# Optimization experiments

Measured on AMD Instinct MI355X. Metric: run time of the kernel, lower is better.

The kernel has to match this reference:

```python
import jax, jax.numpy as jnp
import numpy as np

EPS = 1e-5      # BatchNorm eps (eval mode, running stats at init: mean=0, var=1)
SLOPE = 0.2     # LeakyReLU negative slope


def _knn_idx(x, k):
    # x: (B, N, D) -> (B, N, k) indices of k nearest neighbors (squared L2, feature space)
    sq = jnp.sum(x * x, axis=-1)                              # (B, N)
    dist = sq[:, :, None] + sq[:, None, :] - 2.0 * jnp.einsum('bnd,bmd->bnm', x, x)
    return jax.lax.top_k(-dist, k)[1]                         # nearest = largest of -dist


def _bn_lrelu(y, gamma, beta):
    # eval BatchNorm with running_mean=0, running_var=1, then LeakyReLU(0.2)
    y = y * (gamma / jnp.sqrt(1.0 + EPS)) + beta
    return jnp.where(y >= 0, y, SLOPE * y)


def _edge_conv(x, W, gamma, beta, k):
    # x: (B, N, D); W: (C_out, 2D). Returns (B, N, C_out) after max over k neighbors.
    idx = _knn_idx(x, k)                                      # (B, N, k)
    nb = jax.vmap(lambda xt, i: xt[i])(x, idx)                # (B, N, k, D) neighbor gather
    ctr = jnp.broadcast_to(x[:, :, None, :], nb.shape)
    feat = jnp.concatenate([nb - ctr, ctr], axis=-1)          # (B, N, k, 2D)
    y = jnp.einsum('bnkd,od->bnko', feat, W)                  # 1x1 conv (no bias)
    y = _bn_lrelu(y, gamma, beta)
    return jnp.max(y, axis=2)                                 # max-pool over neighbors


def setup_inputs() -> dict:
    key = jax.random.key(0)
    ks = jax.random.split(key, 16)
    B, N, k, out_dim = 8, 4096, 20, 512
    x = jax.random.normal(ks[0], (B, 3, N), dtype=jnp.float32)
    dims = [(64, 6), (64, 128), (128, 128), (256, 256), (out_dim, 512)]
    inp = {'x': x, 'k': k}
    for i, (co, ci) in enumerate(dims, start=1):
        inp[f'W{i}'] = jax.random.normal(ks[3 * i - 2], (co, ci), dtype=jnp.float32) * (1.0 / np.sqrt(ci))
        inp[f'g{i}'] = jax.random.uniform(ks[3 * i - 1], (co,), dtype=jnp.float32, minval=0.5, maxval=1.5)
        inp[f'b{i}'] = 0.1 * jax.random.normal(ks[3 * i], (co,), dtype=jnp.float32)
    return inp


def reference(x, W1, g1, b1, W2, g2, b2, W3, g3, b3, W4, g4, b4, W5, g5, b5, k):
    xt = jnp.transpose(x, (0, 2, 1))                          # (B, N, 3)
    x1 = _edge_conv(xt, W1, g1, b1, k)                        # (B, N, 64)
    x2 = _edge_conv(x1, W2, g2, b2, k)                        # (B, N, 64)
    x3 = _edge_conv(x2, W3, g3, b3, k)                        # (B, N, 128)
    x4 = _edge_conv(x3, W4, g4, b4, k)                        # (B, N, 256)
    h = jnp.concatenate([x1, x2, x3, x4], axis=-1)            # (B, N, 512)
    y = _bn_lrelu(jnp.einsum('bnd,od->bno', h, W5), g5, b5)   # (B, N, out_dim)
    return jnp.concatenate([jnp.max(y, axis=1), jnp.mean(y, axis=1)], axis=-1)  # (B, 2*out_dim)
```

## Files before the change

### kernel.cpp

```cpp
#include <hip/hip_runtime.h>
#include <math.h>

#define BATCH 8
#define N_PTS 4096
#define KNN 20
#define EPS_BN 1e-5f
#define SLOPE 0.2f
#define M_ROWS (BATCH * N_PTS)

typedef __attribute__((ext_vector_type(8))) short short8;
typedef __attribute__((ext_vector_type(4))) float float4v;

__device__ __forceinline__ unsigned short f2bf(float f) {
    unsigned u = __float_as_uint(f);
    unsigned r = (u + 0x7FFFu + ((u >> 16) & 1u)) >> 16;
    return (unsigned short)r;
}
__device__ __forceinline__ float bf2f(unsigned short h) {
    return __uint_as_float((unsigned)h << 16);
}

__global__ void convert_x1(const float* __restrict__ x,
                           unsigned short* __restrict__ xh, unsigned short* __restrict__ xl,
                           float* __restrict__ sq) {
    int i = blockIdx.x * blockDim.x + threadIdx.x;
    if (i >= M_ROWS) return;
    int b = i / N_PTS, n = i % N_PTS;
    float v[3], s = 0.f;
    #pragma unroll
    for (int d = 0; d < 3; ++d) {
        v[d] = x[((size_t)b * 3 + d) * N_PTS + n];
        s += v[d] * v[d];
    }
    sq[i] = s;
    #pragma unroll
    for (int d = 0; d < 32; ++d) {
        float f = (d < 3) ? v[d] : 0.f;
        unsigned short h = f2bf(f);
        xh[(size_t)i * 32 + d] = h;
        xl[(size_t)i * 32 + d] = f2bf(f - bf2f(h));
    }
}

__global__ void sqnorm_hl(const unsigned short* __restrict__ hh,
                          const unsigned short* __restrict__ hl,
                          int D, float* __restrict__ sq) {
    int w = threadIdx.x >> 6, lane = threadIdx.x & 63;
    int row = blockIdx.x * 4 + w;
    if (row >= M_ROWS) return;
    const unsigned short* ph = hh + (size_t)row * 512;
    const unsigned short* pl = hl + (size_t)row * 512;
    float s = 0.f;
    for (int d = lane; d < D; d += 64) {
        float v = bf2f(ph[d]) + bf2f(pl[d]);
        s += v * v;
    }
    #pragma unroll
    for (int off = 32; off > 0; off >>= 1) s += __shfl_down(s, off, 64);
    if (lane == 0) sq[row] = s;
}

__global__ void repack_edge_split(const float* __restrict__ W, int Co, int D, int KP,
                                  unsigned short* __restrict__ Wh, unsigned short* __restrict__ Wl) {
    int i = blockIdx.x * blockDim.x + threadIdx.x;
    int tot = 2 * Co * KP;
    if (i >= tot) return;
    int r = i / KP, d = i % KP;
    float v = 0.f;
    if (d < D) v = (r < Co) ? W[(size_t)r * 2 * D + d] : W[(size_t)(r - Co) * 2 * D + D + d];
    unsigned short h = f2bf(v);
    Wh[i] = h; Wl[i] = f2bf(v - bf2f(h));
}

__global__ void repack_w5_split(const float* __restrict__ W,
                                unsigned short* __restrict__ Wh, unsigned short* __restrict__ Wl) {
    int i = blockIdx.x * blockDim.x + threadIdx.x;
    if (i >= 512 * 512) return;
    float v = W[i];
    unsigned short h = f2bf(v);
    Wh[i] = h; Wl[i] = f2bf(v - bf2f(h));
}

template<int DPAD>
__launch_bounds__(256, 3)
__global__ void knn_mfma(const unsigned short* __restrict__ Xh,
                         const unsigned short* __restrict__ Xl,
                         int strideX,
                         const float* __restrict__ sq, int* __restrict__ idxout) {
    constexpr int KS  = DPAD / 32;
    constexpr int BST = DPAD + 8;
    constexpr int C8  = DPAD / 8;
    constexpr int SB  = 64 * BST;
    constexpr size_t STAGE = (size_t)2 * SB * 2 + (size_t)64 * 65 * 4 + 64 * 4;
    constexpr size_t MERGE = (size_t)64 * 61 * 4 * 2;
    constexpr size_t POOL  = STAGE > MERGE ? STAGE : MERGE;
    __shared__ __align__(16) char smem[POOL];
    unsigned short* BhS = (unsigned short*)smem;
    unsigned short* BlS = BhS + SB;
    float* Sf  = (float*)(smem + (size_t)2 * SB * 2);
    float* sqs = Sf + 64 * 65;
    float*    kb = (float*)smem;
    unsigned* ib = (unsigned*)(kb + 64 * 61);

    const int b = blockIdx.y;
    const int row0 = blockIdx.x * 64;
    const int tid = threadIdx.x;
    const int w = tid >> 6, lane = tid & 63;
    const int n = lane & 15, q = lane >> 4;
    const int r = tid & 63, t = tid >> 6;

    const unsigned short* Xhb = Xh + (size_t)b * N_PTS * strideX;
    const unsigned short* Xlb = Xl + (size_t)b * N_PTS * strideX;
    const float* sqb = sq + (size_t)b * N_PTS;

    short8 ah[KS], al[KS];
    #pragma unroll
    for (int ks = 0; ks < KS; ++ks) {
        size_t o = (size_t)(row0 + w * 16 + n) * strideX + ks * 32 + q * 8;
        ah[ks] = *(const short8*)(Xhb + o);
        al[ks] = *(const short8*)(Xlb + o);
    }

    float fv[KNN]; int fi[KNN];
    #pragma unroll
    for (int p = 0; p < KNN; ++p) { fv[p] = INFINITY; fi[p] = 0x7FFFFFFF; }

    for (int c0 = 0; c0 < N_PTS; c0 += 64) {
        __syncthreads();
        for (int tt = tid; tt < 64 * C8; tt += 256) {
            int rr = tt / C8, c8 = tt % C8;
            size_t o = (size_t)(c0 + rr) * strideX + c8 * 8;
            *(short8*)&BhS[rr * BST + c8 * 8] = *(const short8*)(Xhb + o);
            *(short8*)&BlS[rr * BST + c8 * 8] = *(const short8*)(Xlb + o);
        }
        if (tid < 64) sqs[tid] = sqb[c0 + tid];
        __syncthreads();

        float4v acc[4];
        #pragma unroll
        for (int ct = 0; ct < 4; ++ct) acc[ct] = (float4v){0.f, 0.f, 0.f, 0.f};

        #pragma unroll
        for (int ks = 0; ks < KS; ++ks) {
            #pragma unroll
            for (int ct = 0; ct < 4; ++ct) {
                short8 bh = *(const short8*)&BhS[(ct * 16 + n) * BST + ks * 32 + q * 8];
                short8 bl = *(const short8*)&BlS[(ct * 16 + n) * BST + ks * 32 + q * 8];
                acc[ct] = __builtin_amdgcn_mfma_f32_16x16x32_bf16(ah[ks], bh, acc[ct], 0, 0, 0);
                acc[ct] = __builtin_amdgcn_mfma_f32_16x16x32_bf16(al[ks], bh, acc[ct], 0, 0, 0);
                acc[ct] = __builtin_amdgcn_mfma_f32_16x16x32_bf16(ah[ks], bl, acc[ct], 0, 0, 0);
            }
        }

        #pragma unroll
        for (int ct = 0; ct < 4; ++ct) {
            int lc = ct * 16 + n;
            int pos = (n & 3) * 16 + ct * 4 + (n >> 2);
            float sc = sqs[lc];
            #pragma unroll
            for (int e = 0; e < 4; ++e)
                Sf[(w * 16 + q * 4 + e) * 65 + pos] = sc - 2.f * acc[ct][e];
        }
        __syncthreads();

        const int sbase = r * 65 + t * 16;
        unsigned mask = 0;
        #pragma unroll
        for (int jj = 0; jj < 16; ++jj) {
            float v = Sf[sbase + jj];
            if (v < fv[KNN - 1]) mask |= (1u << jj);
        }
        while (mask) {
            int jj = __ffs(mask) - 1;
            mask &= mask - 1;
            float v = Sf[sbase + jj];
            if (v < fv[KNN - 1]) {
                fv[KNN - 1] = v;
                fi[KNN - 1] = c0 + (jj << 2) + t;
                #pragma unroll
                for (int p = KNN - 1; p > 0; --p) {
                    float va = fv[p - 1], vb = fv[p];
                    int   ia = fi[p - 1], ic = fi[p];
                    bool sw = vb < va;
                    fv[p - 1] = sw ? vb : va; fv[p] = sw ? va : vb;
                    fi[p - 1] = sw ? ic : ia; fi[p] = sw ? ia : ic;
                }
            }
        }
    }
    __syncthreads();

    if (t > 0) {
        #pragma unroll
        for (int p = 0; p < KNN; ++p) {
            kb[r * 61 + (t - 1) * KNN + p] = fv[p];
            ib[r * 61 + (t - 1) * KNN + p] = (unsigned)fi[p];
        }
    }
    __syncthreads();
    if (tid < 64) {
        #pragma unroll 1
        for (int qq = 0; qq < 3 * KNN; ++qq) {
            float    v  = kb[tid * 61 + qq];
            unsigned ii = ib[tid * 61 + qq];
            bool ins = (v < fv[KNN - 1]) ||
                       (v == fv[KNN - 1] && (int)ii < fi[KNN - 1]);
            if (ins) {
                fv[KNN - 1] = v; fi[KNN - 1] = (int)ii;
                #pragma unroll
                for (int p = KNN - 1; p > 0; --p) {
                    float va = fv[p - 1], vb = fv[p];
                    int   ia = fi[p - 1], ic = fi[p];
                    bool sw = (vb < va) || (vb == va && ic < ia);
                    fv[p - 1] = sw ? vb : va; fv[p] = sw ? va : vb;
                    fi[p - 1] = sw ? ic : ia; fi[p] = sw ? ia : ic;
                }
            }
        }
        int* op = idxout + ((size_t)(b * N_PTS + row0 + tid)) * KNN;
        #pragma unroll
        for (int p = 0; p < KNN; ++p) op[p] = fi[p];
    }
}

__launch_bounds__(256)
__global__ void fgemm(const unsigned short* __restrict__ Ah, const unsigned short* __restrict__ Al,
                      int strideA, int K,
                      const unsigned short* __restrict__ Wh, const unsigned short* __restrict__ Wl,
                      int C, float* __restrict__ out, int fuse_bn,
                      const float* __restrict__ g, const float* __restrict__ beta) {
    __shared__ unsigned short AhS[128 * 40];
    __shared__ unsigned short AlS[128 * 40];
    __shared__ unsigned short BhS[128 * 40];
    __shared__ unsigned short BlS[128 * 40];

    const int c0 = blockIdx.x * 128;
    const int m0 = blockIdx.y * 128;
    const int tid = threadIdx.x;
    const int w = tid >> 6, lane = tid & 63;
    const int n = lane & 15, q = lane >> 4;

    float4v acc[2][8];
    #pragma unroll
    for (int rt = 0; rt < 2; ++rt)
        #pragma unroll
        for (int ct = 0; ct < 8; ++ct) acc[rt][ct] = (float4v){0.f, 0.f, 0.f, 0.f};

    for (int kk = 0; kk < K; kk += 32) {
        __syncthreads();
        for (int tt = tid; tt < 512; tt += 256) {
            int rr = tt >> 2, c8 = tt & 3;
            size_t oa = (size_t)(m0 + rr) * strideA + kk + c8 * 8;
            *(short8*)&AhS[rr * 40 + c8 * 8] = *(const short8*)(Ah + oa);
            *(short8*)&AlS[rr * 40 + c8 * 8] = *(const short8*)(Al + oa);
            size_t ob = (size_t)(c0 + rr) * K + kk + c8 * 8;
            *(short8*)&BhS[rr * 40 + c8 * 8] = *(const short8*)(Wh + ob);
            *(short8*)&BlS[rr * 40 + c8 * 8] = *(const short8*)(Wl + ob);
        }
        __syncthreads();

        short8 af[2][2];
        #pragma unroll
        for (int rt = 0; rt < 2; ++rt) {
            af[rt][0] = *(const short8*)&AhS[(w * 32 + rt * 16 + n) * 40 + q * 8];
            af[rt][1] = *(const short8*)&AlS[(w * 32 + rt * 16 + n) * 40 + q * 8];
        }
        #pragma unroll
        for (int ct = 0; ct < 8; ++ct) {
            short8 bh = *(const short8*)&BhS[(ct * 16 + n) * 40 + q * 8];
            short8 bl = *(const short8*)&BlS[(ct * 16 + n) * 40 + q * 8];
            #pragma unroll
            for (int rt = 0; rt < 2; ++rt) {
                acc[rt][ct] = __builtin_amdgcn_mfma_f32_16x16x32_bf16(af[rt][0], bh, acc[rt][ct], 0, 0, 0);
                acc[rt][ct] = __builtin_amdgcn_mfma_f32_16x16x32_bf16(af[rt][1], bh, acc[rt][ct], 0, 0, 0);
                acc[rt][ct] = __builtin_amdgcn_mfma_f32_16x16x32_bf16(af[rt][0], bl, acc[rt][ct], 0, 0, 0);
            }
        }
    }

    #pragma unroll
    for (int rt = 0; rt < 2; ++rt)
        #pragma unroll
        for (int ct = 0; ct < 8; ++ct) {
            int c = c0 + ct * 16 + n;
            float sc = 1.f, bt = 0.f;
            if (fuse_bn) { sc = g[c] / sqrtf(1.f + EPS_BN); bt = beta[c]; }
            #pragma unroll
            for (int e = 0; e < 4; ++e) {
                int m = m0 + w * 32 + rt * 16 + q * 4 + e;
                float v = acc[rt][ct][e];
                if (fuse_bn) { v = v * sc + bt; v = (v >= 0.f) ? v : SLOPE * v; }
                out[(size_t)m * C + c] = v;
            }
        }
}

__global__ void pool_kernel(const float* __restrict__ zc2, int Co,
                            const int* __restrict__ idx,
                            const float* __restrict__ g, const float* __restrict__ beta,
                            unsigned short* __restrict__ hh, unsigned short* __restrict__ hl,
                            int hoff) {
    int n = blockIdx.x, b = blockIdx.y;
    int o = threadIdx.x;
    size_t bn = (size_t)b * N_PTS + n;
    const int* ip = idx + bn * KNN;
    float zn   = zc2[bn * (size_t)(2 * Co) + o];
    float base = zc2[bn * (size_t)(2 * Co) + Co + o] - zn;
    float m = -INFINITY;
    #pragma unroll
    for (int j = 0; j < KNN; ++j) {
        size_t rr = (size_t)b * N_PTS + ip[j];
        m = fmaxf(m, zc2[rr * (size_t)(2 * Co) + o]);
    }
    float y = m + base;
    float sc = g[o] / sqrtf(1.f + EPS_BN);
    y = y * sc + beta[o];
    y = (y >= 0.f) ? y : SLOPE * y;
    unsigned short h = f2bf(y);
    hh[bn * 512 + hoff + o] = h;
    hl[bn * 512 + hoff + o] = f2bf(y - bf2f(h));
}

__global__ void reduce_partial(const float* __restrict__ y5,
                               float* __restrict__ pmax, float* __restrict__ psum) {
    int chunk = blockIdx.x, b = blockIdx.y, c = threadIdx.x;
    float mx = -INFINITY, sm = 0.f;
    for (int qq = 0; qq < 256; ++qq) {
        int n = chunk * 256 + qq;
        float v = y5[((size_t)b * N_PTS + n) * 512 + c];
        mx = fmaxf(mx, v);
        sm += v;
    }
    pmax[((size_t)b * 16 + chunk) * 512 + c] = mx;
    psum[((size_t)b * 16 + chunk) * 512 + c] = sm;
}

__global__ void reduce_final(const float* __restrict__ pmax,
                             const float* __restrict__ psum,
                             float* __restrict__ out) {
    int i = blockIdx.x * blockDim.x + threadIdx.x;
    if (i >= BATCH * 512) return;
    int b = i / 512, c = i % 512;
    float mx = -INFINITY, sm = 0.f;
    for (int qq = 0; qq < 16; ++qq) {
        mx = fmaxf(mx, pmax[((size_t)b * 16 + qq) * 512 + c]);
        sm += psum[((size_t)b * 16 + qq) * 512 + c];
    }
    out[(size_t)b * 1024 + c] = mx;
    out[(size_t)b * 1024 + 512 + c] = sm * (1.f / 4096.f);
}

extern "C" void kernel_launch(void* const* d_in, const int* in_sizes, int n_in,
                              void* d_out, int out_size, void* d_ws, size_t ws_size,
                              hipStream_t stream) {
    const float* x = (const float*)d_in[0];
    const float* W[5], *gg[5], *bb[5];
    for (int i = 0; i < 5; ++i) {
        W[i]  = (const float*)d_in[2 + 3 * i];
        gg[i] = (const float*)d_in[3 + 3 * i];
        bb[i] = (const float*)d_in[4 + 3 * i];
    }
    float* outp = (float*)d_out;

    char* wsb = (char*)d_ws;
    size_t off = 0;
    unsigned short* x1h = (unsigned short*)(wsb + off); off += (size_t)M_ROWS * 32 * 2;
    unsigned short* x1l = (unsigned short*)(wsb + off); off += (size_t)M_ROWS * 32 * 2;
    float* sq = (float*)(wsb + off); off += (size_t)M_ROWS * 4;
    int*   idx = (int*)(wsb + off); off += (size_t)M_ROWS * KNN * 4;
    unsigned short* Wh = (unsigned short*)(wsb + off); off += (size_t)512 * 512 * 2;
    unsigned short* Wl = (unsigned short*)(wsb + off); off += (size_t)512 * 512 * 2;
    unsigned short* hh = (unsigned short*)(wsb + off); off += (size_t)M_ROWS * 512 * 2;
    unsigned short* hl = (unsigned short*)(wsb + off); off += (size_t)M_ROWS * 512 * 2;
    float* zc2 = (float*)(wsb + off); off += (size_t)M_ROWS * 512 * 4;
    float* pmx = (float*)(wsb + off); off += (size_t)BATCH * 16 * 512 * 4;
    float* psm = (float*)(wsb + off); off += (size_t)BATCH * 16 * 512 * 4;
    (void)ws_size; (void)in_sizes; (void)n_in; (void)out_size;

    convert_x1<<<(M_ROWS + 255) / 256, 256, 0, stream>>>(x, x1h, x1l, sq);

    struct L { int D, Co, KP, hoff; };
    const L layers[4] = { {3, 64, 32, 0}, {64, 64, 64, 64}, {64, 128, 64, 128}, {128, 256, 128, 256} };

    for (int li = 0; li < 4; ++li) {
        const L& ly = layers[li];
        const unsigned short* Ahp;
        const unsigned short* Alp;
        int strideA;
        if (li == 0) { Ahp = x1h; Alp = x1l; strideA = 32; }
        else {
            int po = layers[li - 1].hoff;
            Ahp = hh + po; Alp = hl + po; strideA = 512;
            sqnorm_hl<<<M_ROWS / 4, 256, 0, stream>>>(Ahp, Alp, ly.D, sq);
        }

        if (li == 0)
            knn_mfma<32><<<dim3(N_PTS / 64, BATCH), 256, 0, stream>>>(Ahp, Alp, strideA, sq, idx);
        else if (ly.D == 64)
            knn_mfma<64><<<dim3(N_PTS / 64, BATCH), 256, 0, stream>>>(Ahp, Alp, strideA, sq, idx);
        else
            knn_mfma<128><<<dim3(N_PTS / 64, BATCH), 256, 0, stream>>>(Ahp, Alp, strideA, sq, idx);

        repack_edge_split<<<(2 * ly.Co * ly.KP + 255) / 256, 256, 0, stream>>>(
            W[li], ly.Co, ly.D, ly.KP, Wh, Wl);
        fgemm<<<dim3((2 * ly.Co) / 128, M_ROWS / 128), 256, 0, stream>>>(
            Ahp, Alp, strideA, ly.KP, Wh, Wl, 2 * ly.Co, zc2, 0, nullptr, nullptr);
        pool_kernel<<<dim3(N_PTS, BATCH), ly.Co, 0, stream>>>(
            zc2, ly.Co, idx, gg[li], bb[li], hh, hl, ly.hoff);
    }

    repack_w5_split<<<(512 * 512 + 255) / 256, 256, 0, stream>>>(W[4], Wh, Wl);
    fgemm<<<dim3(4, M_ROWS / 128), 256, 0, stream>>>(
        hh, hl, 512, 512, Wh, Wl, 512, zc2, 1, gg[4], bb[4]);

    reduce_partial<<<dim3(16, BATCH), 512, 0, stream>>>(zc2, pmx, psm);
    reduce_final<<<(BATCH * 512 + 255) / 256, 256, 0, stream>>>(pmx, psm, outp);
}
```

Baseline: 1.585 ms.

## Switch kNN distance tile to 32x32x16 MFMA with XOR-swizzled LDS layout

The kNN kernel's 64x64 distance tile now uses 32x32x16 bf16 MFMA, with each wave owning a 32x32 sub-tile, in place of four 16x16x32 MFMAs per wave. The candidate tile is staged into LDS without padding, using an XOR swizzle on 8-element chunks to avoid bank conflicts. This is meant to cut LDS operand reads per MFMA and improve matrix-core throughput, but it lowers the launch_bounds occupancy hint from 3 to 2 blocks. Separately, the final reduction is split into 32 chunks per batch instead of 16 to give it more parallelism.

```diff
diff --git a/kernel.cpp b/kernel.cpp
--- a/kernel.cpp
+++ b/kernel.cpp
@@ -10,6 +10,7 @@
 
 typedef __attribute__((ext_vector_type(8))) short short8;
 typedef __attribute__((ext_vector_type(4))) float float4v;
+typedef __attribute__((ext_vector_type(16))) float float16v;
 
 __device__ __forceinline__ unsigned short f2bf(float f) {
     unsigned u = __float_as_uint(f);
@@ -82,15 +83,15 @@
 }
 
 template<int DPAD>
-__launch_bounds__(256, 3)
+__launch_bounds__(256, 2)
 __global__ void knn_mfma(const unsigned short* __restrict__ Xh,
                          const unsigned short* __restrict__ Xl,
                          int strideX,
                          const float* __restrict__ sq, int* __restrict__ idxout) {
-    constexpr int KS  = DPAD / 32;
-    constexpr int BST = DPAD + 8;
-    constexpr int C8  = DPAD / 8;
-    constexpr int SB  = 64 * BST;
+    constexpr int KS16 = DPAD / 16;
+    constexpr int C8   = DPAD / 8;
+    constexpr int XK   = (C8 - 1) < 7 ? (C8 - 1) : 7;
+    constexpr int SB   = 64 * DPAD;
     constexpr size_t STAGE = (size_t)2 * SB * 2 + (size_t)64 * 65 * 4 + 64 * 4;
     constexpr size_t MERGE = (size_t)64 * 61 * 4 * 2;
     constexpr size_t POOL  = STAGE > MERGE ? STAGE : MERGE;
@@ -106,17 +107,19 @@
     const int row0 = blockIdx.x * 64;
     const int tid = threadIdx.x;
     const int w = tid >> 6, lane = tid & 63;
-    const int n = lane & 15, q = lane >> 4;
+    const int l31 = lane & 31, lh = lane >> 5;
     const int r = tid & 63, t = tid >> 6;
+    const int rbase = (w & 1) * 32;
+    const int cb32  = (w >> 1) * 32;
 
     const unsigned short* Xhb = Xh + (size_t)b * N_PTS * strideX;
     const unsigned short* Xlb = Xl + (size_t)b * N_PTS * strideX;
     const float* sqb = sq + (size_t)b * N_PTS;
 
-    short8 ah[KS], al[KS];
-    #pragma unroll
-    for (int ks = 0; ks < KS; ++ks) {
-        size_t o = (size_t)(row0 + w * 16 + n) * strideX + ks * 32 + q * 8;
+    short8 ah[KS16], al[KS16];
+    #pragma unroll
+    for (int ks = 0; ks < KS16; ++ks) {
+        size_t o = (size_t)(row0 + rbase + l31) * strideX + ks * 16 + lh * 8;
         ah[ks] = *(const short8*)(Xhb + o);
         al[ks] = *(const short8*)(Xlb + o);
     }
@@ -127,39 +130,40 @@
 
     for (int c0 = 0; c0 < N_PTS; c0 += 64) {
         __syncthreads();
-        for (int tt = tid; tt < 64 * C8; tt += 256) {
-            int rr = tt / C8, c8 = tt % C8;
-            size_t o = (size_t)(c0 + rr) * strideX + c8 * 8;
-            *(short8*)&BhS[rr * BST + c8 * 8] = *(const short8*)(Xhb + o);
-            *(short8*)&BlS[rr * BST + c8 * 8] = *(const short8*)(Xlb + o);
+        #pragma unroll
+        for (int it = 0; it < (64 * C8 + 255) / 256; ++it) {
+            int tt = tid + it * 256;
+            int col = tt / C8, kcs = tt % C8;
+            int kcg = kcs ^ (col & XK);
+            size_t o = (size_t)(c0 + col) * strideX + kcg * 8;
+            *(short8*)&BhS[tt * 8] = *(const short8*)(Xhb + o);
+            *(short8*)&BlS[tt * 8] = *(const short8*)(Xlb + o);
         }
         if (tid < 64) sqs[tid] = sqb[c0 + tid];
         __syncthreads();
 
-        float4v acc[4];
-        #pragma unroll
-        for (int ct = 0; ct < 4; ++ct) acc[ct] = (float4v){0.f, 0.f, 0.f, 0.f};
-
-        #pragma unroll
-        for (int ks = 0; ks < KS; ++ks) {
+        float16v acc = {};
+
+        const int colL = cb32 + l31;
+        const int cbase_us = colL * DPAD;
+        #pragma unroll
+        for (int ks = 0; ks < KS16; ++ks) {
+            int ch = ((ks * 2 + lh) ^ (colL & XK)) * 8;
+            short8 bh = *(const short8*)&BhS[cbase_us + ch];
+            short8 bl = *(const short8*)&BlS[cbase_us + ch];
+            acc = __builtin_amdgcn_mfma_f32_32x32x16_bf16(ah[ks], bh, acc, 0, 0, 0);
+            acc = __builtin_amdgcn_mfma_f32_32x32x16_bf16(al[ks], bh, acc, 0, 0, 0);
+            acc = __builtin_amdgcn_mfma_f32_32x32x16_bf16(ah[ks], bl, acc, 0, 0, 0);
+        }
+
+        {
+            float sc = sqs[colL];
+            int pos = (colL & 3) * 16 + (colL >> 2);
             #pragma unroll
-            for (int ct = 0; ct < 4; ++ct) {
-                short8 bh = *(const short8*)&BhS[(ct * 16 + n) * BST + ks * 32 + q * 8];
-                short8 bl = *(const short8*)&BlS[(ct * 16 + n) * BST + ks * 32 + q * 8];
-                acc[ct] = __builtin_amdgcn_mfma_f32_16x16x32_bf16(ah[ks], bh, acc[ct], 0, 0, 0);
-                acc[ct] = __builtin_amdgcn_mfma_f32_16x16x32_bf16(al[ks], bh, acc[ct], 0, 0, 0);
-                acc[ct] = __builtin_amdgcn_mfma_f32_16x16x32_bf16(ah[ks], bl, acc[ct], 0, 0, 0);
+            for (int reg = 0; reg < 16; ++reg) {
+                int rowL = rbase + (reg & 3) + 8 * (reg >> 2) + 4 * lh;
+                Sf[rowL * 65 + pos] = sc - 2.f * acc[reg];
             }
-        }
-
-        #pragma unroll
-        for (int ct = 0; ct < 4; ++ct) {
-            int lc = ct * 16 + n;
-            int pos = (n & 3) * 16 + ct * 4 + (n >> 2);
-            float sc = sqs[lc];
-            #pragma unroll
-            for (int e = 0; e < 4; ++e)
-                Sf[(w * 16 + q * 4 + e) * 65 + pos] = sc - 2.f * acc[ct][e];
         }
         __syncthreads();
 
@@ -325,14 +329,14 @@
                                float* __restrict__ pmax, float* __restrict__ psum) {
     int chunk = blockIdx.x, b = blockIdx.y, c = threadIdx.x;
     float mx = -INFINITY, sm = 0.f;
-    for (int qq = 0; qq < 256; ++qq) {
-        int n = chunk * 256 + qq;
+    for (int qq = 0; qq < 128; ++qq) {
+        int n = chunk * 128 + qq;
         float v = y5[((size_t)b * N_PTS + n) * 512 + c];
         mx = fmaxf(mx, v);
         sm += v;
     }
-    pmax[((size_t)b * 16 + chunk) * 512 + c] = mx;
-    psum[((size_t)b * 16 + chunk) * 512 + c] = sm;
+    pmax[((size_t)b * 32 + chunk) * 512 + c] = mx;
+    psum[((size_t)b * 32 + chunk) * 512 + c] = sm;
 }
 
 __global__ void reduce_final(const float* __restrict__ pmax,
@@ -342,9 +346,9 @@
     if (i >= BATCH * 512) return;
     int b = i / 512, c = i % 512;
     float mx = -INFINITY, sm = 0.f;
-    for (int qq = 0; qq < 16; ++qq) {
-        mx = fmaxf(mx, pmax[((size_t)b * 16 + qq) * 512 + c]);
-        sm += psum[((size_t)b * 16 + qq) * 512 + c];
+    for (int qq = 0; qq < 32; ++qq) {
+        mx = fmaxf(mx, pmax[((size_t)b * 32 + qq) * 512 + c]);
+        sm += psum[((size_t)b * 32 + qq) * 512 + c];
     }
     out[(size_t)b * 1024 + c] = mx;
     out[(size_t)b * 1024 + 512 + c] = sm * (1.f / 4096.f);
@@ -373,8 +377,8 @@
     unsigned short* hh = (unsigned short*)(wsb + off); off += (size_t)M_ROWS * 512 * 2;
     unsigned short* hl = (unsigned short*)(wsb + off); off += (size_t)M_ROWS * 512 * 2;
     float* zc2 = (float*)(wsb + off); off += (size_t)M_ROWS * 512 * 4;
-    float* pmx = (float*)(wsb + off); off += (size_t)BATCH * 16 * 512 * 4;
-    float* psm = (float*)(wsb + off); off += (size_t)BATCH * 16 * 512 * 4;
+    float* pmx = (float*)(wsb + off); off += (size_t)BATCH * 32 * 512 * 4;
+    float* psm = (float*)(wsb + off); off += (size_t)BATCH * 32 * 512 * 4;
     (void)ws_size; (void)in_sizes; (void)n_in; (void)out_size;
 
     convert_x1<<<(M_ROWS + 255) / 256, 256, 0, stream>>>(x, x1h, x1l, sq);
@@ -413,6 +417,6 @@
     fgemm<<<dim3(4, M_ROWS / 128), 256, 0, stream>>>(
         hh, hl, 512, 512, Wh, Wl, 512, zc2, 1, gg[4], bb[4]);
 
-    reduce_partial<<<dim3(16, BATCH), 512, 0, stream>>>(zc2, pmx, psm);
+    reduce_partial<<<dim3(32, BATCH), 512, 0, stream>>>(zc2, pmx, psm);
     reduce_final<<<(BATCH * 512 + 255) / 256, 256, 0, stream>>>(pmx, psm, outp);
 }
```

New measurement: 1.459 ms. 7.9% less time.
